# Performance work log

Hardware: AMD Instinct MI355X
Metric: run time of the kernel (lower is better)

The kernel has to match this reference:

```python
import jax, jax.numpy as jnp
import numpy as np

B, D, HID = 16384, 1024, 4096
HALF = D // 2


def setup_inputs() -> dict:
    key = jax.random.key(0)
    ks = jax.random.split(key, 9)
    sc_in = 1.0 / np.sqrt(HALF)
    sc_h = 1.0 / np.sqrt(HID)
    return {
        "z": jax.random.normal(ks[0], (B, D), dtype=jnp.float32),
        "W1s": jax.random.uniform(ks[1], (HALF, HID), jnp.float32, -sc_in, sc_in),
        "b1s": jax.random.uniform(ks[2], (HID,), jnp.float32, -sc_in, sc_in),
        "W2s": jax.random.uniform(ks[3], (HID, HALF), jnp.float32, -sc_h, sc_h),
        "b2s": jax.random.uniform(ks[4], (HALF,), jnp.float32, -sc_h, sc_h),
        "W1t": jax.random.uniform(ks[5], (HALF, HID), jnp.float32, -sc_in, sc_in),
        "b1t": jax.random.uniform(ks[6], (HID,), jnp.float32, -sc_in, sc_in),
        "W2t": jax.random.uniform(ks[7], (HID, HALF), jnp.float32, -sc_h, sc_h),
        "b2t": jax.random.uniform(ks[8], (HALF,), jnp.float32, -sc_h, sc_h),
    }


def reference(z, W1s, b1s, W2s, b2s, W1t, b1t, W2t, b2t):
    # mask_even=True: a = even-indexed features, b = odd-indexed features
    a = z[:, 0::2]  # [B, HALF]
    b = z[:, 1::2]  # [B, HALF]
    # two-layer MLPs for s and t (cond=None -> inp = a)
    s = jnp.maximum(a @ W1s + b1s, 0.0) @ W2s + b2s  # [B, HALF]
    t = jnp.maximum(a @ W1t + b1t, 0.0) @ W2t + b2t  # [B, HALF]
    b_out = b * jnp.exp(s) + t
    logdet = s.sum(axis=1)  # [B]
    # scatter back: a -> even slots, b_out -> odd slots (interleave)
    z_out = jnp.stack([a, b_out], axis=-1).reshape(z.shape)
    return z_out, logdet
```

## Files before the change

kernel.cpp:

```cpp
#include <hip/hip_runtime.h>
#include <hip/hip_bf16.h>
#include <cstdint>
#include <cstddef>

#define BROWS  16384
#define DDIM   1024
#define HID_N  4096
#define HALF_K 512
#define LDH    8192

typedef __attribute__((ext_vector_type(8))) short s8v;
typedef __attribute__((ext_vector_type(4))) float f4v;

__device__ __forceinline__ void gload16(const void* g, void* l) {
  __builtin_amdgcn_global_load_lds(
      (const __attribute__((address_space(1))) unsigned int*)g,
      (__attribute__((address_space(3))) unsigned int*)l, 16, 0, 0);
}
#define BAR() asm volatile("s_barrier" ::: "memory")

template <int N> __device__ __forceinline__ void vmw() {
  if constexpr (N == 0)      asm volatile("s_waitcnt vmcnt(0)" ::: "memory");
  else if constexpr (N == 3) asm volatile("s_waitcnt vmcnt(3)" ::: "memory");
  else                       asm volatile("s_waitcnt vmcnt(4)" ::: "memory");
}

__global__ __launch_bounds__(256) void cast_a_kernel(const float* __restrict__ z,
                                                     __hip_bfloat16* __restrict__ a16) {
  const int idx = blockIdx.x * 256 + threadIdx.x;
  const int m  = idx >> 6;
  const int kb = idx & 63;
  const float4* zp = (const float4*)(z + (size_t)m * DDIM + (size_t)kb * 16);
  alignas(16) __hip_bfloat16 t[8];
#pragma unroll
  for (int i = 0; i < 4; ++i) {
    float4 v = zp[i];
    t[2 * i]     = __float2bfloat16(v.x);
    t[2 * i + 1] = __float2bfloat16(v.z);
  }
  *(s8v*)(a16 + (size_t)m * HALF_K + kb * 8) = *(const s8v*)t;
}

__global__ __launch_bounds__(256) void transpose_cast_kernel(const float* __restrict__ W,
                                                             __hip_bfloat16* __restrict__ WT,
                                                             int K, int N) {
  __shared__ float tile[32][33];
  const int n0 = blockIdx.x * 32, k0 = blockIdx.y * 32;
  const int tx = threadIdx.x & 31;
  const int ty = threadIdx.x >> 5;
#pragma unroll
  for (int i = 0; i < 32; i += 8)
    tile[ty + i][tx] = W[(size_t)(k0 + ty + i) * N + n0 + tx];
  __syncthreads();
#pragma unroll
  for (int i = 0; i < 32; i += 8)
    WT[(size_t)(n0 + ty + i) * K + k0 + tx] = __float2bfloat16(tile[tx][ty + i]);
}

template <int NREP, int EPI>
__global__ __launch_bounds__(512, 2)
void gemm8_kernel(const __hip_bfloat16* A0p, const __hip_bfloat16* BT0,
                  const float* __restrict__ bias00, const float* __restrict__ bias01,
                  int nsplit, int K, int lda, int ldb,
                  __hip_bfloat16* __restrict__ Hout,
                  float* Fout0, int ldo,
                  const __hip_bfloat16* A1p, const __hip_bfloat16* BT1,
                  const float* bias10, float* Fout1) {
  constexpr int BN    = 64 * NREP;
  constexpr int BHALF = (BN / 2) * 128;
  constexpr int BUF   = 32768 + 2 * BHALF;
  __shared__ char smem[2 * BUF];

  const __hip_bfloat16* A  = A0p;
  const __hip_bfloat16* Bt = BT0;
  const float* bias0 = bias00;
  float* Fout = Fout0;
  if (EPI == 1 && blockIdx.z) { A = A1p; Bt = BT1; bias0 = bias10; Fout = Fout1; }

  const int tid = threadIdx.x;
  const int m0 = blockIdx.x * 256;
  const int n0 = blockIdx.y * BN;

  const int trow = tid >> 3;
  const int scol = ((tid & 7) * 16) ^ ((trow & 7) << 4);
  const char* Ab = (const char*)A;
  const char* Bb = (const char*)Bt;
  const size_t ldab = (size_t)lda * 2, ldbb = (size_t)ldb * 2;
  const int NT = K >> 6;

  const int lane = tid & 63, wid = tid >> 6;
  const int wr = wid >> 2, wc = wid & 3;
  const int lr = lane & 15, lk = lane >> 4;
  const int xo = (lr & 7) << 4;

  int aoff[4][2], boff[NREP / 2][2];
#pragma unroll
  for (int j = 0; j < 4; ++j)
#pragma unroll
    for (int kk = 0; kk < 2; ++kk)
      aoff[j][kk] = (j * 32 + wr * 16 + lr) * 128 + ((kk * 64 + lk * 16) ^ xo);
#pragma unroll
  for (int nn = 0; nn < NREP / 2; ++nn)
#pragma unroll
    for (int kk = 0; kk < 2; ++kk)
      boff[nn][kk] = (nn * 64 + wc * 16 + lr) * 128 + ((kk * 64 + lk * 16) ^ xo);

  f4v acc[8][NREP] = {};

  auto stage_A = [&](int h, int T) {
#pragma unroll
    for (int l = 0; l < 2; ++l)
      gload16(Ab + (size_t)(m0 + h * 128 + l * 64 + trow) * ldab + (size_t)T * 128 + scol,
              smem + (T & 1) * BUF + h * 16384 + l * 8192 + tid * 16);
  };
  auto stage_B = [&](int h, int T) {
#pragma unroll
    for (int l = 0; l < NREP / 2; ++l)
      gload16(Bb + (size_t)(n0 + h * (BN / 2) + l * 64 + trow) * ldbb + (size_t)T * 128 + scol,
              smem + (T & 1) * BUF + 32768 + h * BHALF + l * 8192 + tid * 16);
  };

  stage_A(0, 0); stage_A(1, 0); stage_B(0, 0); stage_B(1, 0);
  if (NT > 1) { stage_A(0, 1); stage_B(0, 1); vmw<2 + NREP / 2>(); }
  else        { vmw<0>(); }
  BAR();

  for (int T = 0; T < NT; ++T) {
    const char* bufp = smem + (T & 1) * BUF;
    s8v af[4][2], bfr[NREP / 2][2];

#pragma unroll
    for (int j = 0; j < 4; ++j) {
      af[j][0] = *(const s8v*)(bufp + aoff[j][0]);
      af[j][1] = *(const s8v*)(bufp + aoff[j][1]);
    }
#pragma unroll
    for (int nn = 0; nn < NREP / 2; ++nn) {
      bfr[nn][0] = *(const s8v*)(bufp + 32768 + boff[nn][0]);
      bfr[nn][1] = *(const s8v*)(bufp + 32768 + boff[nn][1]);
    }
    if (T + 1 < NT) stage_B(1, T + 1);
    BAR();
    __builtin_amdgcn_sched_barrier(0);
    __builtin_amdgcn_s_setprio(1);
#pragma unroll
    for (int j = 0; j < 4; ++j)
#pragma unroll
      for (int nn = 0; nn < NREP / 2; ++nn)
#pragma unroll
        for (int kk = 0; kk < 2; ++kk)
          acc[j][nn] = __builtin_amdgcn_mfma_f32_16x16x32_bf16(af[j][kk], bfr[nn][kk], acc[j][nn], 0, 0, 0);
    __builtin_amdgcn_s_setprio(0);
    BAR();

#pragma unroll
    for (int nn = 0; nn < NREP / 2; ++nn) {
      bfr[nn][0] = *(const s8v*)(bufp + 32768 + BHALF + boff[nn][0]);
      bfr[nn][1] = *(const s8v*)(bufp + 32768 + BHALF + boff[nn][1]);
    }
    if (T + 1 < NT) stage_A(1, T + 1);
    BAR();
    __builtin_amdgcn_sched_barrier(0);
    __builtin_amdgcn_s_setprio(1);
#pragma unroll
    for (int j = 0; j < 4; ++j)
#pragma unroll
      for (int nn = 0; nn < NREP / 2; ++nn)
#pragma unroll
        for (int kk = 0; kk < 2; ++kk)
          acc[j][NREP / 2 + nn] = __builtin_amdgcn_mfma_f32_16x16x32_bf16(af[j][kk], bfr[nn][kk], acc[j][NREP / 2 + nn], 0, 0, 0);
    __builtin_amdgcn_s_setprio(0);
    BAR();

#pragma unroll
    for (int j = 0; j < 4; ++j) {
      af[j][0] = *(const s8v*)(bufp + 16384 + aoff[j][0]);
      af[j][1] = *(const s8v*)(bufp + 16384 + aoff[j][1]);
    }
#pragma unroll
    for (int nn = 0; nn < NREP / 2; ++nn) {
      bfr[nn][0] = *(const s8v*)(bufp + 32768 + boff[nn][0]);
      bfr[nn][1] = *(const s8v*)(bufp + 32768 + boff[nn][1]);
    }
    if (T + 2 < NT) stage_A(0, T + 2);
    BAR();
    __builtin_amdgcn_sched_barrier(0);
    __builtin_amdgcn_s_setprio(1);
#pragma unroll
    for (int j = 0; j < 4; ++j)
#pragma unroll
      for (int nn = 0; nn < NREP / 2; ++nn)
#pragma unroll
        for (int kk = 0; kk < 2; ++kk)
          acc[4 + j][nn] = __builtin_amdgcn_mfma_f32_16x16x32_bf16(af[j][kk], bfr[nn][kk], acc[4 + j][nn], 0, 0, 0);
    __builtin_amdgcn_s_setprio(0);
    BAR();

#pragma unroll
    for (int nn = 0; nn < NREP / 2; ++nn) {
      bfr[nn][0] = *(const s8v*)(bufp + 32768 + BHALF + boff[nn][0]);
      bfr[nn][1] = *(const s8v*)(bufp + 32768 + BHALF + boff[nn][1]);
    }
    if (T + 2 < NT) stage_B(0, T + 2);
    BAR();
    __builtin_amdgcn_sched_barrier(0);
    __builtin_amdgcn_s_setprio(1);
#pragma unroll
    for (int j = 0; j < 4; ++j)
#pragma unroll
      for (int nn = 0; nn < NREP / 2; ++nn)
#pragma unroll
        for (int kk = 0; kk < 2; ++kk)
          acc[4 + j][NREP / 2 + nn] = __builtin_amdgcn_mfma_f32_16x16x32_bf16(af[j][kk], bfr[nn][kk], acc[4 + j][NREP / 2 + nn], 0, 0, 0);
    __builtin_amdgcn_s_setprio(0);
    if (T + 2 >= NT) vmw<0>(); else vmw<2 + NREP / 2>();
    BAR();
  }

#pragma unroll
  for (int ni = 0; ni < NREP; ++ni) {
    const int c = n0 + ni * 64 + wc * 16 + lr;
    const float bv = (EPI == 0 && c >= nsplit) ? bias01[c - nsplit] : bias0[EPI == 0 && c >= nsplit ? 0 : c];
#pragma unroll
    for (int mi = 0; mi < 8; ++mi) {
#pragma unroll
      for (int r = 0; r < 4; ++r) {
        const int rr = m0 + mi * 32 + wr * 16 + lk * 4 + r;
        float v = acc[mi][ni][r] + bv;
        if (EPI == 0) {
          Hout[(size_t)rr * LDH + c] = __float2bfloat16(fmaxf(v, 0.0f));
        } else {
          Fout[(size_t)rr * ldo + c] = v;
        }
      }
    }
  }
}

__global__ __launch_bounds__(256) void finish_kernel(const float* __restrict__ z,
                                                     const float* __restrict__ s,
                                                     const float* __restrict__ t,
                                                     float* __restrict__ zout,
                                                     float* __restrict__ ld) {
  const int row = blockIdx.x;
  const int tid = threadIdx.x;
  const float* zr = z + (size_t)row * DDIM;
  float* zo = zout + (size_t)row * DDIM;
  const float* sr = s + (size_t)row * 512;
  const float* tr = t + (size_t)row * 512;
  float acc = 0.0f;
#pragma unroll
  for (int i = 0; i < 2; ++i) {
    const int j = tid + i * 256;
    float2 zv = *(const float2*)(zr + 2 * j);
    float sv = sr[j], tv = tr[j];
    acc += sv;
    float2 o;
    o.x = zv.x;
    o.y = zv.y * expf(sv) + tv;
    *(float2*)(zo + 2 * j) = o;
  }
#pragma unroll
  for (int o = 32; o > 0; o >>= 1) acc += __shfl_down(acc, o, 64);
  __shared__ float w4[4];
  if ((tid & 63) == 0) w4[tid >> 6] = acc;
  __syncthreads();
  if (tid == 0) ld[row] = w4[0] + w4[1] + w4[2] + w4[3];
}

extern "C" void kernel_launch(void* const* d_in, const int* in_sizes, int n_in,
                              void* d_out, int out_size, void* d_ws, size_t ws_size,
                              hipStream_t stream) {
  const float* z   = (const float*)d_in[0];
  const float* W1s = (const float*)d_in[1];
  const float* b1s = (const float*)d_in[2];
  const float* W2s = (const float*)d_in[3];
  const float* b2s = (const float*)d_in[4];
  const float* W1t = (const float*)d_in[5];
  const float* b1t = (const float*)d_in[6];
  const float* W2t = (const float*)d_in[7];
  const float* b2t = (const float*)d_in[8];
  float* zout = (float*)d_out;
  float* ld   = zout + (size_t)BROWS * DDIM;

  char* ws = (char*)d_ws;
  __hip_bfloat16* a16    = (__hip_bfloat16*)ws;
  __hip_bfloat16* w1catT = (__hip_bfloat16*)(ws + 16777216);
  __hip_bfloat16* w2sT   = (__hip_bfloat16*)(ws + 25165824);
  __hip_bfloat16* w2tT   = (__hip_bfloat16*)(ws + 29360128);
  float*          st0    = (float*)(ws + 33554432);
  float*          st1    = (float*)(ws + 67108864);
  char*           hbase  = ws + 100663296;

  int CH = 256;
  for (int c = 16384; c >= 256; c >>= 1) {
    if (100663296ull + (size_t)c * 16384ull <= ws_size) { CH = c; break; }
  }
  __hip_bfloat16* H = (__hip_bfloat16*)hbase;

  cast_a_kernel<<<BROWS * (HALF_K / 8) / 256, 256, 0, stream>>>(z, a16);
  transpose_cast_kernel<<<dim3(128, 16), 256, 0, stream>>>(W1s, w1catT, HALF_K, HID_N);
  transpose_cast_kernel<<<dim3(128, 16), 256, 0, stream>>>(W1t, w1catT + (size_t)HID_N * HALF_K, HALF_K, HID_N);
  transpose_cast_kernel<<<dim3(16, 128), 256, 0, stream>>>(W2s, w2sT, HID_N, HALF_K);
  transpose_cast_kernel<<<dim3(16, 128), 256, 0, stream>>>(W2t, w2tT, HID_N, HALF_K);

  for (int mb = 0; mb < BROWS; mb += CH) {
    gemm8_kernel<4, 0><<<dim3(CH / 256, 32, 1), 512, 0, stream>>>(
        a16 + (size_t)mb * HALF_K, w1catT, b1s, b1t, HID_N,
        HALF_K, HALF_K, HALF_K, H, nullptr, 0, nullptr, nullptr, nullptr, nullptr);
    gemm8_kernel<2, 1><<<dim3(CH / 256, 4, 2), 512, 0, stream>>>(
        H, w2sT, b2s, nullptr, 1 << 30,
        HID_N, LDH, HID_N, nullptr, st0 + (size_t)mb * HALF_K, HALF_K,
        H + HID_N, w2tT, b2t, st1 + (size_t)mb * HALF_K);
  }
  finish_kernel<<<BROWS, 256, 0, stream>>>(z, st0, st1, zout, ld);
}
```

Measured before the change: 387.1 us.

## Fuse coupling epilogue into second GEMM, specialize GEMM kernels, stage H stores via LDS

Splits the templated GEMM into specialized first-layer and second-layer kernels. The second-layer kernel computes s and t together in one workgroup (128-row tiles), applying exp, affine coupling, interleaved output and per-tile logdet partials in its epilogue. This removes the fp32 s/t intermediate buffers and the separate finish pass. The first-layer kernel now writes H through a swizzled LDS staging buffer for coalesced 16-byte stores. Both kernels use a grouped block-index remap for L2 locality, and the minimum chunk size grows. A small reduction kernel sums the logdet partials. The cost is smaller M tiles in GEMM2 with fewer MFMAs per loaded byte, plus the fast __expf approximation.

```diff
diff --git a/kernel.cpp b/kernel.cpp
--- a/kernel.cpp
+++ b/kernel.cpp
@@ -17,12 +17,14 @@
       (const __attribute__((address_space(1))) unsigned int*)g,
       (__attribute__((address_space(3))) unsigned int*)l, 16, 0, 0);
 }
-#define BAR() asm volatile("s_barrier" ::: "memory")
+#define BAR()   asm volatile("s_barrier" ::: "memory")
+#define BARS()  asm volatile("s_waitcnt lgkmcnt(0)\n\ts_barrier" ::: "memory")
+#define SCHED0() __builtin_amdgcn_sched_barrier(0)
 
 template <int N> __device__ __forceinline__ void vmw() {
   if constexpr (N == 0)      asm volatile("s_waitcnt vmcnt(0)" ::: "memory");
-  else if constexpr (N == 3) asm volatile("s_waitcnt vmcnt(3)" ::: "memory");
-  else                       asm volatile("s_waitcnt vmcnt(4)" ::: "memory");
+  else if constexpr (N == 4) asm volatile("s_waitcnt vmcnt(4)" ::: "memory");
+  else if constexpr (N == 8) asm volatile("s_waitcnt vmcnt(8)" ::: "memory");
 }
 
 __global__ __launch_bounds__(256) void cast_a_kernel(const float* __restrict__ z,
@@ -57,77 +59,64 @@
     WT[(size_t)(n0 + ty + i) * K + k0 + tx] = __float2bfloat16(tile[tx][ty + i]);
 }
 
-template <int NREP, int EPI>
 __global__ __launch_bounds__(512, 2)
-void gemm8_kernel(const __hip_bfloat16* A0p, const __hip_bfloat16* BT0,
-                  const float* __restrict__ bias00, const float* __restrict__ bias01,
-                  int nsplit, int K, int lda, int ldb,
-                  __hip_bfloat16* __restrict__ Hout,
-                  float* Fout0, int ldo,
-                  const __hip_bfloat16* A1p, const __hip_bfloat16* BT1,
-                  const float* bias10, float* Fout1) {
-  constexpr int BN    = 64 * NREP;
-  constexpr int BHALF = (BN / 2) * 128;
-  constexpr int BUF   = 32768 + 2 * BHALF;
-  __shared__ char smem[2 * BUF];
-
-  const __hip_bfloat16* A  = A0p;
-  const __hip_bfloat16* Bt = BT0;
-  const float* bias0 = bias00;
-  float* Fout = Fout0;
-  if (EPI == 1 && blockIdx.z) { A = A1p; Bt = BT1; bias0 = bias10; Fout = Fout1; }
+void gemm1_kernel(const __hip_bfloat16* __restrict__ A,
+                  const __hip_bfloat16* __restrict__ BT,
+                  const float* __restrict__ b1s, const float* __restrict__ b1t,
+                  __hip_bfloat16* __restrict__ Hout) {
+  __shared__ alignas(16) char smem[131072];
+  constexpr int NT = HALF_K / 64;
+
+  const int nwg = gridDim.x;
+  const int orig = blockIdx.x;
+  const int vid = (orig & 7) * (nwg >> 3) + (orig >> 3);
+  const int bx = vid >> 5, by = vid & 31;
+  const int m0 = bx * 256, n0 = by * 256;
 
   const int tid = threadIdx.x;
-  const int m0 = blockIdx.x * 256;
-  const int n0 = blockIdx.y * BN;
-
   const int trow = tid >> 3;
   const int scol = ((tid & 7) * 16) ^ ((trow & 7) << 4);
-  const char* Ab = (const char*)A;
-  const char* Bb = (const char*)Bt;
-  const size_t ldab = (size_t)lda * 2, ldbb = (size_t)ldb * 2;
-  const int NT = K >> 6;
 
   const int lane = tid & 63, wid = tid >> 6;
   const int wr = wid >> 2, wc = wid & 3;
   const int lr = lane & 15, lk = lane >> 4;
   const int xo = (lr & 7) << 4;
 
-  int aoff[4][2], boff[NREP / 2][2];
+  int aoff[4][2], boff[2][2];
 #pragma unroll
   for (int j = 0; j < 4; ++j)
 #pragma unroll
     for (int kk = 0; kk < 2; ++kk)
       aoff[j][kk] = (j * 32 + wr * 16 + lr) * 128 + ((kk * 64 + lk * 16) ^ xo);
 #pragma unroll
-  for (int nn = 0; nn < NREP / 2; ++nn)
+  for (int nn = 0; nn < 2; ++nn)
 #pragma unroll
     for (int kk = 0; kk < 2; ++kk)
       boff[nn][kk] = (nn * 64 + wc * 16 + lr) * 128 + ((kk * 64 + lk * 16) ^ xo);
 
-  f4v acc[8][NREP] = {};
+  f4v acc[8][4] = {};
 
   auto stage_A = [&](int h, int T) {
 #pragma unroll
     for (int l = 0; l < 2; ++l)
-      gload16(Ab + (size_t)(m0 + h * 128 + l * 64 + trow) * ldab + (size_t)T * 128 + scol,
-              smem + (T & 1) * BUF + h * 16384 + l * 8192 + tid * 16);
+      gload16((const char*)A + (size_t)(m0 + h * 128 + l * 64 + trow) * (HALF_K * 2) + (size_t)T * 128 + scol,
+              smem + (T & 1) * 65536 + h * 16384 + l * 8192 + tid * 16);
   };
   auto stage_B = [&](int h, int T) {
 #pragma unroll
-    for (int l = 0; l < NREP / 2; ++l)
-      gload16(Bb + (size_t)(n0 + h * (BN / 2) + l * 64 + trow) * ldbb + (size_t)T * 128 + scol,
-              smem + (T & 1) * BUF + 32768 + h * BHALF + l * 8192 + tid * 16);
-  };
-
-  stage_A(0, 0); stage_A(1, 0); stage_B(0, 0); stage_B(1, 0);
-  if (NT > 1) { stage_A(0, 1); stage_B(0, 1); vmw<2 + NREP / 2>(); }
-  else        { vmw<0>(); }
+    for (int l = 0; l < 2; ++l)
+      gload16((const char*)BT + (size_t)(n0 + h * 128 + l * 64 + trow) * (HALF_K * 2) + (size_t)T * 128 + scol,
+              smem + (T & 1) * 65536 + 32768 + h * 16384 + l * 8192 + tid * 16);
+  };
+
+  stage_A(0, 0); stage_B(0, 0); stage_A(1, 0); stage_B(1, 0);
+  stage_A(0, 1); stage_B(0, 1);
+  vmw<4>();
   BAR();
 
   for (int T = 0; T < NT; ++T) {
-    const char* bufp = smem + (T & 1) * BUF;
-    s8v af[4][2], bfr[NREP / 2][2];
+    const char* bufp = smem + (T & 1) * 65536;
+    s8v af[4][2], b0r[2][2], b1r[2][2];
 
 #pragma unroll
     for (int j = 0; j < 4; ++j) {
@@ -135,40 +124,38 @@
       af[j][1] = *(const s8v*)(bufp + aoff[j][1]);
     }
 #pragma unroll
-    for (int nn = 0; nn < NREP / 2; ++nn) {
-      bfr[nn][0] = *(const s8v*)(bufp + 32768 + boff[nn][0]);
-      bfr[nn][1] = *(const s8v*)(bufp + 32768 + boff[nn][1]);
+    for (int nn = 0; nn < 2; ++nn) {
+      b0r[nn][0] = *(const s8v*)(bufp + 32768 + boff[nn][0]);
+      b0r[nn][1] = *(const s8v*)(bufp + 32768 + boff[nn][1]);
     }
     if (T + 1 < NT) stage_B(1, T + 1);
-    BAR();
-    __builtin_amdgcn_sched_barrier(0);
-    __builtin_amdgcn_s_setprio(1);
-#pragma unroll
-    for (int j = 0; j < 4; ++j)
-#pragma unroll
-      for (int nn = 0; nn < NREP / 2; ++nn)
-#pragma unroll
-        for (int kk = 0; kk < 2; ++kk)
-          acc[j][nn] = __builtin_amdgcn_mfma_f32_16x16x32_bf16(af[j][kk], bfr[nn][kk], acc[j][nn], 0, 0, 0);
-    __builtin_amdgcn_s_setprio(0);
-    BAR();
-
-#pragma unroll
-    for (int nn = 0; nn < NREP / 2; ++nn) {
-      bfr[nn][0] = *(const s8v*)(bufp + 32768 + BHALF + boff[nn][0]);
-      bfr[nn][1] = *(const s8v*)(bufp + 32768 + BHALF + boff[nn][1]);
+    BAR(); SCHED0();
+    __builtin_amdgcn_s_setprio(1);
+#pragma unroll
+    for (int j = 0; j < 4; ++j)
+#pragma unroll
+      for (int nn = 0; nn < 2; ++nn)
+#pragma unroll
+        for (int kk = 0; kk < 2; ++kk)
+          acc[j][nn] = __builtin_amdgcn_mfma_f32_16x16x32_bf16(af[j][kk], b0r[nn][kk], acc[j][nn], 0, 0, 0);
+    __builtin_amdgcn_s_setprio(0);
+    BAR();
+
+#pragma unroll
+    for (int nn = 0; nn < 2; ++nn) {
+      b1r[nn][0] = *(const s8v*)(bufp + 49152 + boff[nn][0]);
+      b1r[nn][1] = *(const s8v*)(bufp + 49152 + boff[nn][1]);
     }
     if (T + 1 < NT) stage_A(1, T + 1);
-    BAR();
-    __builtin_amdgcn_sched_barrier(0);
-    __builtin_amdgcn_s_setprio(1);
-#pragma unroll
-    for (int j = 0; j < 4; ++j)
-#pragma unroll
-      for (int nn = 0; nn < NREP / 2; ++nn)
-#pragma unroll
-        for (int kk = 0; kk < 2; ++kk)
-          acc[j][NREP / 2 + nn] = __builtin_amdgcn_mfma_f32_16x16x32_bf16(af[j][kk], bfr[nn][kk], acc[j][NREP / 2 + nn], 0, 0, 0);
+    BAR(); SCHED0();
+    __builtin_amdgcn_s_setprio(1);
+#pragma unroll
+    for (int j = 0; j < 4; ++j)
+#pragma unroll
+      for (int nn = 0; nn < 2; ++nn)
+#pragma unroll
+        for (int kk = 0; kk < 2; ++kk)
+          acc[j][2 + nn] = __builtin_amdgcn_mfma_f32_16x16x32_bf16(af[j][kk], b1r[nn][kk], acc[j][2 + nn], 0, 0, 0);
     __builtin_amdgcn_s_setprio(0);
     BAR();
 
@@ -177,95 +164,243 @@
       af[j][0] = *(const s8v*)(bufp + 16384 + aoff[j][0]);
       af[j][1] = *(const s8v*)(bufp + 16384 + aoff[j][1]);
     }
-#pragma unroll
-    for (int nn = 0; nn < NREP / 2; ++nn) {
+    if (T + 2 < NT) stage_A(0, T + 2);
+    BAR(); SCHED0();
+    __builtin_amdgcn_s_setprio(1);
+#pragma unroll
+    for (int j = 0; j < 4; ++j)
+#pragma unroll
+      for (int nn = 0; nn < 2; ++nn)
+#pragma unroll
+        for (int kk = 0; kk < 2; ++kk)
+          acc[4 + j][nn] = __builtin_amdgcn_mfma_f32_16x16x32_bf16(af[j][kk], b0r[nn][kk], acc[4 + j][nn], 0, 0, 0);
+    __builtin_amdgcn_s_setprio(0);
+    BAR();
+
+    if (T + 2 < NT) stage_B(0, T + 2);
+    SCHED0();
+    __builtin_amdgcn_s_setprio(1);
+#pragma unroll
+    for (int j = 0; j < 4; ++j)
+#pragma unroll
+      for (int nn = 0; nn < 2; ++nn)
+#pragma unroll
+        for (int kk = 0; kk < 2; ++kk)
+          acc[4 + j][2 + nn] = __builtin_amdgcn_mfma_f32_16x16x32_bf16(af[j][kk], b1r[nn][kk], acc[4 + j][2 + nn], 0, 0, 0);
+    __builtin_amdgcn_s_setprio(0);
+    if (T + 2 >= NT) vmw<0>(); else vmw<4>();
+    BAR();
+  }
+
+  const float* bp = (n0 < HID_N) ? b1s : b1t;
+  const int cb0 = n0 & (HID_N - 1);
+  float bv[4];
+#pragma unroll
+  for (int ni = 0; ni < 4; ++ni) bv[ni] = bp[cb0 + ni * 64 + wc * 16 + lr];
+  const int rbase = wr * 16 + lk * 4;
+
+#pragma unroll
+  for (int mi = 0; mi < 8; ++mi) {
+    BARS();
+#pragma unroll
+    for (int ni = 0; ni < 4; ++ni) {
+      const int cb = (ni * 64 + wc * 16 + lr) * 2;
+#pragma unroll
+      for (int r = 0; r < 4; ++r) {
+        const int row = rbase + r;
+        float v = fmaxf(acc[mi][ni][r] + bv[ni], 0.0f);
+        *(__hip_bfloat16*)(smem + row * 512 + (cb ^ ((row & 7) << 4))) = __float2bfloat16(v);
+      }
+    }
+    BARS();
+#pragma unroll
+    for (int i = 0; i < 2; ++i) {
+      const int bo = tid * 32 + i * 16;
+      const int row = bo >> 9, cb = bo & 511;
+      s8v v = *(const s8v*)(smem + row * 512 + (cb ^ ((row & 7) << 4)));
+      *(s8v*)((char*)Hout + ((size_t)(m0 + mi * 32 + row) * LDH + n0) * 2 + cb) = v;
+    }
+  }
+}
+
+__global__ __launch_bounds__(512, 2)
+void gemm2_kernel(const __hip_bfloat16* __restrict__ H,
+                  const __hip_bfloat16* __restrict__ BsT,
+                  const __hip_bfloat16* __restrict__ BtT,
+                  const float* __restrict__ b2s, const float* __restrict__ b2t,
+                  const float* __restrict__ zin, float* __restrict__ zout,
+                  float* __restrict__ gpart) {
+  __shared__ alignas(16) char smem[131072];
+  constexpr int NT = HID_N / 64;
+
+  const int nwg = gridDim.x;
+  const int orig = blockIdx.x;
+  const int vid = (orig & 7) * (nwg >> 3) + (orig >> 3);
+  const int rb = vid >> 2, by = vid & 3;
+  const int m0 = rb * 128, n0c = by * 128;
+
+  const int tid = threadIdx.x;
+  const int trow = tid >> 3;
+  const int scol = ((tid & 7) * 16) ^ ((trow & 7) << 4);
+
+  const int lane = tid & 63, wid = tid >> 6;
+  const int wr = wid >> 2, wc = wid & 3;
+  const int lr = lane & 15, lk = lane >> 4;
+  const int xo = (lr & 7) << 4;
+
+  int aoff[4][2], boff[2][2];
+#pragma unroll
+  for (int j = 0; j < 4; ++j)
+#pragma unroll
+    for (int kk = 0; kk < 2; ++kk)
+      aoff[j][kk] = (j * 32 + wr * 16 + lr) * 128 + ((kk * 64 + lk * 16) ^ xo);
+#pragma unroll
+  for (int nn = 0; nn < 2; ++nn)
+#pragma unroll
+    for (int kk = 0; kk < 2; ++kk)
+      boff[nn][kk] = (nn * 64 + wc * 16 + lr) * 128 + ((kk * 64 + lk * 16) ^ xo);
+
+  f4v as[4][2] = {}, at[4][2] = {};
+
+  auto stage_As = [&](int T) {
+#pragma unroll
+    for (int l = 0; l < 2; ++l)
+      gload16((const char*)H + (size_t)(m0 + l * 64 + trow) * (LDH * 2) + (size_t)T * 128 + scol,
+              smem + (T & 1) * 65536 + l * 8192 + tid * 16);
+  };
+  auto stage_At = [&](int T) {
+#pragma unroll
+    for (int l = 0; l < 2; ++l)
+      gload16((const char*)H + (size_t)(m0 + l * 64 + trow) * (LDH * 2) + 8192 + (size_t)T * 128 + scol,
+              smem + (T & 1) * 65536 + 16384 + l * 8192 + tid * 16);
+  };
+  auto stage_Bs = [&](int T) {
+#pragma unroll
+    for (int l = 0; l < 2; ++l)
+      gload16((const char*)BsT + (size_t)(n0c + l * 64 + trow) * (HID_N * 2) + (size_t)T * 128 + scol,
+              smem + (T & 1) * 65536 + 32768 + l * 8192 + tid * 16);
+  };
+  auto stage_Bt = [&](int T) {
+#pragma unroll
+    for (int l = 0; l < 2; ++l)
+      gload16((const char*)BtT + (size_t)(n0c + l * 64 + trow) * (HID_N * 2) + (size_t)T * 128 + scol,
+              smem + (T & 1) * 65536 + 49152 + l * 8192 + tid * 16);
+  };
+
+  stage_As(0); stage_Bs(0); stage_At(0); stage_Bt(0); stage_As(1); stage_Bs(1);
+  vmw<8>();
+  BAR();
+
+  for (int T = 0; T < NT; ++T) {
+    const char* bufp = smem + (T & 1) * 65536;
+    s8v af[4][2], bfr[2][2];
+
+#pragma unroll
+    for (int j = 0; j < 4; ++j) {
+      af[j][0] = *(const s8v*)(bufp + aoff[j][0]);
+      af[j][1] = *(const s8v*)(bufp + aoff[j][1]);
+    }
+#pragma unroll
+    for (int nn = 0; nn < 2; ++nn) {
       bfr[nn][0] = *(const s8v*)(bufp + 32768 + boff[nn][0]);
       bfr[nn][1] = *(const s8v*)(bufp + 32768 + boff[nn][1]);
     }
-    if (T + 2 < NT) stage_A(0, T + 2);
-    BAR();
-    __builtin_amdgcn_sched_barrier(0);
-    __builtin_amdgcn_s_setprio(1);
-#pragma unroll
-    for (int j = 0; j < 4; ++j)
-#pragma unroll
-      for (int nn = 0; nn < NREP / 2; ++nn)
-#pragma unroll
-        for (int kk = 0; kk < 2; ++kk)
-          acc[4 + j][nn] = __builtin_amdgcn_mfma_f32_16x16x32_bf16(af[j][kk], bfr[nn][kk], acc[4 + j][nn], 0, 0, 0);
-    __builtin_amdgcn_s_setprio(0);
-    BAR();
-
-#pragma unroll
-    for (int nn = 0; nn < NREP / 2; ++nn) {
-      bfr[nn][0] = *(const s8v*)(bufp + 32768 + BHALF + boff[nn][0]);
-      bfr[nn][1] = *(const s8v*)(bufp + 32768 + BHALF + boff[nn][1]);
-    }
-    if (T + 2 < NT) stage_B(0, T + 2);
-    BAR();
-    __builtin_amdgcn_sched_barrier(0);
-    __builtin_amdgcn_s_setprio(1);
-#pragma unroll
-    for (int j = 0; j < 4; ++j)
-#pragma unroll
-      for (int nn = 0; nn < NREP / 2; ++nn)
-#pragma unroll
-        for (int kk = 0; kk < 2; ++kk)
-          acc[4 + j][NREP / 2 + nn] = __builtin_amdgcn_mfma_f32_16x16x32_bf16(af[j][kk], bfr[nn][kk], acc[4 + j][NREP / 2 + nn], 0, 0, 0);
-    __builtin_amdgcn_s_setprio(0);
-    if (T + 2 >= NT) vmw<0>(); else vmw<2 + NREP / 2>();
-    BAR();
-  }
-
-#pragma unroll
-  for (int ni = 0; ni < NREP; ++ni) {
-    const int c = n0 + ni * 64 + wc * 16 + lr;
-    const float bv = (EPI == 0 && c >= nsplit) ? bias01[c - nsplit] : bias0[EPI == 0 && c >= nsplit ? 0 : c];
-#pragma unroll
-    for (int mi = 0; mi < 8; ++mi) {
+    if (T + 1 < NT) { stage_At(T + 1); stage_Bt(T + 1); }
+    BAR(); SCHED0();
+    __builtin_amdgcn_s_setprio(1);
+#pragma unroll
+    for (int j = 0; j < 4; ++j)
+#pragma unroll
+      for (int nn = 0; nn < 2; ++nn)
+#pragma unroll
+        for (int kk = 0; kk < 2; ++kk)
+          as[j][nn] = __builtin_amdgcn_mfma_f32_16x16x32_bf16(af[j][kk], bfr[nn][kk], as[j][nn], 0, 0, 0);
+    __builtin_amdgcn_s_setprio(0);
+    if (T + 1 >= NT) vmw<0>(); else vmw<8>();
+    BAR();
+
+#pragma unroll
+    for (int j = 0; j < 4; ++j) {
+      af[j][0] = *(const s8v*)(bufp + 16384 + aoff[j][0]);
+      af[j][1] = *(const s8v*)(bufp + 16384 + aoff[j][1]);
+    }
+#pragma unroll
+    for (int nn = 0; nn < 2; ++nn) {
+      bfr[nn][0] = *(const s8v*)(bufp + 49152 + boff[nn][0]);
+      bfr[nn][1] = *(const s8v*)(bufp + 49152 + boff[nn][1]);
+    }
+    if (T + 2 < NT) { stage_As(T + 2); stage_Bs(T + 2); }
+    BAR(); SCHED0();
+    __builtin_amdgcn_s_setprio(1);
+#pragma unroll
+    for (int j = 0; j < 4; ++j)
+#pragma unroll
+      for (int nn = 0; nn < 2; ++nn)
+#pragma unroll
+        for (int kk = 0; kk < 2; ++kk)
+          at[j][nn] = __builtin_amdgcn_mfma_f32_16x16x32_bf16(af[j][kk], bfr[nn][kk], at[j][nn], 0, 0, 0);
+    __builtin_amdgcn_s_setprio(0);
+    if (T + 2 >= NT) vmw<0>(); else vmw<8>();
+    BAR();
+  }
+
+  float bvs[2], bvt[2];
+#pragma unroll
+  for (int ni = 0; ni < 2; ++ni) {
+    const int c = n0c + ni * 64 + wc * 16 + lr;
+    bvs[ni] = b2s[c];
+    bvt[ni] = b2t[c];
+  }
+  float pl[4][4] = {};
+#pragma unroll
+  for (int mi = 0; mi < 4; ++mi) {
+#pragma unroll
+    for (int ni = 0; ni < 2; ++ni) {
+      const int cg = n0c + ni * 64 + wc * 16 + lr;
 #pragma unroll
       for (int r = 0; r < 4; ++r) {
         const int rr = m0 + mi * 32 + wr * 16 + lk * 4 + r;
-        float v = acc[mi][ni][r] + bv;
-        if (EPI == 0) {
-          Hout[(size_t)rr * LDH + c] = __float2bfloat16(fmaxf(v, 0.0f));
-        } else {
-          Fout[(size_t)rr * ldo + c] = v;
-        }
+        const float sv = as[mi][ni][r] + bvs[ni];
+        const float tv = at[mi][ni][r] + bvt[ni];
+        pl[mi][r] += sv;
+        const size_t base = (size_t)rr * DDIM + 2 * cg;
+        float2 zv = *(const float2*)(zin + base);
+        float2 o;
+        o.x = zv.x;
+        o.y = zv.y * __expf(sv) + tv;
+        *(float2*)(zout + base) = o;
       }
     }
   }
-}
-
-__global__ __launch_bounds__(256) void finish_kernel(const float* __restrict__ z,
-                                                     const float* __restrict__ s,
-                                                     const float* __restrict__ t,
-                                                     float* __restrict__ zout,
-                                                     float* __restrict__ ld) {
-  const int row = blockIdx.x;
-  const int tid = threadIdx.x;
-  const float* zr = z + (size_t)row * DDIM;
-  float* zo = zout + (size_t)row * DDIM;
-  const float* sr = s + (size_t)row * 512;
-  const float* tr = t + (size_t)row * 512;
-  float acc = 0.0f;
-#pragma unroll
-  for (int i = 0; i < 2; ++i) {
-    const int j = tid + i * 256;
-    float2 zv = *(const float2*)(zr + 2 * j);
-    float sv = sr[j], tv = tr[j];
-    acc += sv;
-    float2 o;
-    o.x = zv.x;
-    o.y = zv.y * expf(sv) + tv;
-    *(float2*)(zo + 2 * j) = o;
-  }
-#pragma unroll
-  for (int o = 32; o > 0; o >>= 1) acc += __shfl_down(acc, o, 64);
-  __shared__ float w4[4];
-  if ((tid & 63) == 0) w4[tid >> 6] = acc;
-  __syncthreads();
-  if (tid == 0) ld[row] = w4[0] + w4[1] + w4[2] + w4[3];
+#pragma unroll
+  for (int m = 1; m < 16; m <<= 1)
+#pragma unroll
+    for (int mi = 0; mi < 4; ++mi)
+#pragma unroll
+      for (int r = 0; r < 4; ++r)
+        pl[mi][r] += __shfl_xor(pl[mi][r], m, 64);
+
+  float (*ldp)[4] = (float (*)[4])smem;
+  BARS();
+  if (lr == 0) {
+#pragma unroll
+    for (int mi = 0; mi < 4; ++mi)
+#pragma unroll
+      for (int r = 0; r < 4; ++r)
+        ldp[mi * 32 + wr * 16 + lk * 4 + r][wc] = pl[mi][r];
+  }
+  BARS();
+  if (tid < 128) {
+    float v = ldp[tid][0] + ldp[tid][1] + ldp[tid][2] + ldp[tid][3];
+    gpart[(size_t)(m0 + tid) * 4 + by] = v;
+  }
+}
+
+__global__ __launch_bounds__(256) void ld_reduce_kernel(const float* __restrict__ gpart,
+                                                        float* __restrict__ ld) {
+  const int r = blockIdx.x * 256 + threadIdx.x;
+  float4 v = ((const float4*)gpart)[r];
+  ld[r] = v.x + v.y + v.z + v.w;
 }
 
 extern "C" void kernel_launch(void* const* d_in, const int* in_sizes, int n_in,
@@ -288,13 +423,12 @@
   __hip_bfloat16* w1catT = (__hip_bfloat16*)(ws + 16777216);
   __hip_bfloat16* w2sT   = (__hip_bfloat16*)(ws + 25165824);
   __hip_bfloat16* w2tT   = (__hip_bfloat16*)(ws + 29360128);
-  float*          st0    = (float*)(ws + 33554432);
-  float*          st1    = (float*)(ws + 67108864);
-  char*           hbase  = ws + 100663296;
-
-  int CH = 256;
-  for (int c = 16384; c >= 256; c >>= 1) {
-    if (100663296ull + (size_t)c * 16384ull <= ws_size) { CH = c; break; }
+  float*          gpart  = (float*)(ws + 33554432);
+  char*           hbase  = ws + 33816576;
+
+  int CH = 2048;
+  for (int c = 8192; c >= 2048; c >>= 1) {
+    if (33816576ull + (size_t)c * 16384ull <= ws_size) { CH = c; break; }
   }
   __hip_bfloat16* H = (__hip_bfloat16*)hbase;
 
@@ -305,13 +439,11 @@
   transpose_cast_kernel<<<dim3(16, 128), 256, 0, stream>>>(W2t, w2tT, HID_N, HALF_K);
 
   for (int mb = 0; mb < BROWS; mb += CH) {
-    gemm8_kernel<4, 0><<<dim3(CH / 256, 32, 1), 512, 0, stream>>>(
-        a16 + (size_t)mb * HALF_K, w1catT, b1s, b1t, HID_N,
-        HALF_K, HALF_K, HALF_K, H, nullptr, 0, nullptr, nullptr, nullptr, nullptr);
-    gemm8_kernel<2, 1><<<dim3(CH / 256, 4, 2), 512, 0, stream>>>(
-        H, w2sT, b2s, nullptr, 1 << 30,
-        HID_N, LDH, HID_N, nullptr, st0 + (size_t)mb * HALF_K, HALF_K,
-        H + HID_N, w2tT, b2t, st1 + (size_t)mb * HALF_K);
-  }
-  finish_kernel<<<BROWS, 256, 0, stream>>>(z, st0, st1, zout, ld);
-}
+    gemm1_kernel<<<(CH / 256) * 32, 512, 0, stream>>>(
+        a16 + (size_t)mb * HALF_K, w1catT, b1s, b1t, H);
+    gemm2_kernel<<<(CH / 128) * 4, 512, 0, stream>>>(
+        H, w2sT, w2tT, b2s, b2t,
+        z + (size_t)mb * DDIM, zout + (size_t)mb * DDIM, gpart + (size_t)mb * 4);
+  }
+  ld_reduce_kernel<<<BROWS / 256, 256, 0, stream>>>(gpart, ld);
+}
```

Result: faster. 370.4 us (-4.3%).
